# Kernel optimization log

Measured on AMD Instinct MI355X. Metric: run time of the kernel, lower is better.

The kernel has to match this reference:

```python
import jax, jax.numpy as jnp
import numpy as np
import math

HID = 128
NH = 8
HD = HID // NH
NL = 3
CLIP = 10.0
EPS = 1e-5

def _ln(x, g, b):
    mu = jnp.mean(x, axis=-1, keepdims=True)
    var = jnp.var(x, axis=-1, keepdims=True)
    return (x - mu) * jax.lax.rsqrt(var + EPS) * g + b

def _layer(h, e_bias1, e_gate2, g1, b1, wh, g2, b2, w1, w2):
    B, N, _ = h.shape
    h_in = h
    hn = _ln(h, g1, b1)
    qkv = hn @ wh                                   # (B,N,3H)
    q, k, v = jnp.split(qkv, 3, axis=-1)
    q = q.reshape(B, N, NH, HD).transpose(0, 2, 1, 3)  # (B,nh,N,hd)
    k = k.reshape(B, N, NH, HD).transpose(0, 2, 1, 3)
    v = v.reshape(B, N, NH, HD).transpose(0, 2, 1, 3)
    att = jnp.einsum('bhid,bhjd->bhij', q, k) * (1.0 / math.sqrt(HD))
    att = jax.nn.softmax(att + e_bias1, axis=-1) * e_gate2
    y = jnp.einsum('bhij,bhjd->bhid', att, v)
    y = y.transpose(0, 2, 1, 3).reshape(B, N, HID)
    z = _ln(y + h_in, g2, b2)
    mlp = jax.nn.relu(z @ w1) @ w2
    return mlp + y

def setup_inputs() -> dict:
    key = jax.random.key(0)
    ks = jax.random.split(key, 9)
    d = {
        'node_features': jax.random.normal(ks[0], (16, 256, 2), jnp.float32),
        'edge_features': jax.random.normal(ks[1], (16, 256, 256, 1), jnp.float32),
        'Wn': jax.random.normal(ks[2], (2, HID), jnp.float32) * 0.5,
        'We_in': jax.random.normal(ks[3], (1, HID), jnp.float32) * 0.1,
        'ln1_g': jnp.ones((NL, HID), jnp.float32),
        'ln1_b': jnp.zeros((NL, HID), jnp.float32),
        'Wh': jax.random.normal(ks[4], (NL, HID, 3 * HID), jnp.float32) * (1.0 / math.sqrt(HID)),
        'We': jax.random.normal(ks[5], (NL, HID, 2 * NH), jnp.float32) * (1.0 / math.sqrt(HID)),
        'ln2_g': jnp.ones((NL, HID), jnp.float32),
        'ln2_b': jnp.zeros((NL, HID), jnp.float32),
        'W1': jax.random.normal(ks[6], (NL, HID, 4 * HID), jnp.float32) * (1.0 / math.sqrt(HID)),
        'W2': jax.random.normal(ks[7], (NL, 4 * HID, HID), jnp.float32) * (1.0 / math.sqrt(4 * HID)),
        'Wdec': jax.random.normal(ks[8], (HID, 1), jnp.float32) * (1.0 / math.sqrt(HID)),
    }
    return d

def reference(node_features, edge_features, Wn, We_in, ln1_g, ln1_b, Wh, We, ln2_g, ln2_b, W1, W2, Wdec):
    h = node_features @ Wn                              # (B,N,H)
    e = edge_features @ We_in                           # (B,N,N,H)
    for i in range(NL):
        ee = e @ We[i]                                  # (B,N,N,2*nh)
        ee = ee.transpose(0, 3, 1, 2)                   # (B,2*nh,N,N)
        e1, e2 = ee[:, :NH], ee[:, NH:]
        h = _layer(h, e1, e2, ln1_g[i], ln1_b[i], Wh[i], ln2_g[i], ln2_b[i], W1[i], W2[i])
    out = h @ Wdec                                      # (B,N,1)
    out = CLIP * jnp.tanh(out / math.sqrt(HID))
    return out
```

## Files before the change

kernel.cpp:

```cpp
#include <hip/hip_runtime.h>
#include <math.h>

#define HID 128
#define NHEAD 8
#define NL 3
#define NS 256
#define ROWS 4096

typedef __attribute__((ext_vector_type(8))) short bf16x8;
typedef __attribute__((ext_vector_type(4))) float f32x4;

__device__ __forceinline__ float us2f(unsigned short s) { return __uint_as_float(((unsigned)s) << 16); }
__device__ __forceinline__ unsigned short f2b(float f) {
    unsigned u = __float_as_uint(f);
    return (unsigned short)((u + 0x7fff + ((u >> 16) & 1)) >> 16);
}

__global__ __launch_bounds__(256) void k_prep(
    const float* __restrict__ Wh, const float* __restrict__ W1, const float* __restrict__ W2,
    const float* __restrict__ We_in, const float* __restrict__ We,
    const float* __restrict__ nf, const float* __restrict__ Wn,
    unsigned short* __restrict__ WhH, unsigned short* __restrict__ WhL,
    unsigned short* __restrict__ W1H, unsigned short* __restrict__ W1L,
    unsigned short* __restrict__ W2H, unsigned short* __restrict__ W2L,
    float* __restrict__ sbuf, float* __restrict__ h)
{
    int b = blockIdx.x, t = threadIdx.x;
    if (b >= 529) {
        int idx = (b - 529) * 256 + t;
        int r = idx >> 7, c = idx & 127;
        h[idx] = nf[2 * r] * Wn[c] + nf[2 * r + 1] * Wn[HID + c];
        return;
    }
    if (b == 528) {
        if (t < NL * 2 * NHEAD) {
            int l = t / (2 * NHEAD), j = t % (2 * NHEAD);
            float acc = 0.f;
            for (int c = 0; c < HID; ++c)
                acc += We_in[c] * We[(long)(l * HID + c) * (2 * NHEAD) + j];
            sbuf[t] = acc;
        }
        return;
    }
    const float* S; unsigned short *OH, *OL; int K, N, kt, nt;
    if (b < 144) {
        int l = b / 48, rem = b % 48; kt = rem & 3; nt = rem >> 2; K = 128; N = 384;
        S = Wh + (long)l * 128 * 384; OH = WhH + (long)l * 384 * 128; OL = WhL + (long)l * 384 * 128;
    } else if (b < 336) {
        int b2 = b - 144; int l = b2 / 64, rem = b2 % 64; kt = rem & 3; nt = rem >> 2; K = 128; N = 512;
        S = W1 + (long)l * 128 * 512; OH = W1H + (long)l * 512 * 128; OL = W1L + (long)l * 512 * 128;
    } else {
        int b2 = b - 336; int l = b2 / 64, rem = b2 % 64; kt = rem & 15; nt = rem >> 4; K = 512; N = 128;
        S = W2 + (long)l * 512 * 128; OH = W2H + (long)l * 128 * 512; OL = W2L + (long)l * 128 * 512;
    }
    __shared__ float sm[32][33];
    int i0 = t >> 5, j = t & 31;
#pragma unroll
    for (int p = 0; p < 4; ++p) {
        int i = i0 + p * 8;
        sm[i][j] = S[(long)(kt * 32 + i) * N + nt * 32 + j];
    }
    __syncthreads();
#pragma unroll
    for (int p = 0; p < 4; ++p) {
        int n = i0 + p * 8;
        float v = sm[j][n];
        unsigned short hh = f2b(v);
        long o = (long)(nt * 32 + n) * K + kt * 32 + j;
        OH[o] = hh; OL[o] = f2b(v - us2f(hh));
    }
}

__global__ __launch_bounds__(256) void k_fgemm(
    const float* __restrict__ x, const float* __restrict__ x2,
    const float* __restrict__ g, const float* __restrict__ b,
    const unsigned short* __restrict__ WH, const unsigned short* __restrict__ WL,
    unsigned short* __restrict__ Ch, unsigned short* __restrict__ Cl,
    int mode)
{
    __shared__ unsigned short sAh[64 * 136], sAl[64 * 136];
    __shared__ unsigned short sWh[64 * 136], sWl[64 * 136];
    int t = threadIdx.x;
    int row0 = blockIdx.y * 64, col0 = blockIdx.x * 64;

#pragma unroll
    for (int p = 0; p < 4; ++p) {
        int rr = (t >> 4) + p * 16, ck = t & 15;
        *(uint4*)&sWh[rr * 136 + ck * 8] = *(const uint4*)&WH[(long)(col0 + rr) * 128 + ck * 8];
        *(uint4*)&sWl[rr * 136 + ck * 8] = *(const uint4*)&WL[(long)(col0 + rr) * 128 + ck * 8];
    }
#pragma unroll
    for (int pass = 0; pass < 2; ++pass) {
        int row = pass * 32 + (t >> 3);
        int p = t & 7, cb = p * 16;
        float v[16];
        const float* xp = x + (long)(row0 + row) * HID + cb;
#pragma unroll
        for (int j = 0; j < 16; j += 4) *(float4*)&v[j] = *(const float4*)(xp + j);
        if (x2) {
            const float* yp = x2 + (long)(row0 + row) * HID + cb;
#pragma unroll
            for (int j = 0; j < 16; j += 4) {
                float4 r4 = *(const float4*)(yp + j);
                v[j] += r4.x; v[j+1] += r4.y; v[j+2] += r4.z; v[j+3] += r4.w;
            }
        }
        float s = 0.f, s2 = 0.f;
#pragma unroll
        for (int j = 0; j < 16; ++j) { s += v[j]; s2 += v[j] * v[j]; }
        s  += __shfl_xor(s, 1);  s  += __shfl_xor(s, 2);  s  += __shfl_xor(s, 4);
        s2 += __shfl_xor(s2, 1); s2 += __shfl_xor(s2, 2); s2 += __shfl_xor(s2, 4);
        float mu  = s * (1.f / HID);
        float var = s2 * (1.f / HID) - mu * mu;
        float inv = rsqrtf(var + 1e-5f);
        unsigned short hi[16], lo[16];
#pragma unroll
        for (int j = 0; j < 16; ++j) {
            int c = cb + j;
            float o = (v[j] - mu) * inv * g[c] + b[c];
            hi[j] = f2b(o); lo[j] = f2b(o - us2f(hi[j]));
        }
        *(uint4*)&sAh[row * 136 + cb]     = *(uint4*)&hi[0];
        *(uint4*)&sAh[row * 136 + cb + 8] = *(uint4*)&hi[8];
        *(uint4*)&sAl[row * 136 + cb]     = *(uint4*)&lo[0];
        *(uint4*)&sAl[row * 136 + cb + 8] = *(uint4*)&lo[8];
    }
    __syncthreads();

    int w = t >> 6, lane = t & 63;
    int m = lane & 15, quad = lane >> 4;
    f32x4 acc[4];
#pragma unroll
    for (int i = 0; i < 4; ++i) acc[i] = (f32x4){0.f, 0.f, 0.f, 0.f};
#pragma unroll
    for (int c = 0; c < 4; ++c) {
        bf16x8 ah = *(const bf16x8*)&sAh[(w * 16 + m) * 136 + c * 32 + quad * 8];
        bf16x8 al = *(const bf16x8*)&sAl[(w * 16 + m) * 136 + c * 32 + quad * 8];
#pragma unroll
        for (int nt = 0; nt < 4; ++nt) {
            bf16x8 wh = *(const bf16x8*)&sWh[(nt * 16 + m) * 136 + c * 32 + quad * 8];
            bf16x8 wl = *(const bf16x8*)&sWl[(nt * 16 + m) * 136 + c * 32 + quad * 8];
            acc[nt] = __builtin_amdgcn_mfma_f32_16x16x32_bf16(ah, wh, acc[nt], 0, 0, 0);
            acc[nt] = __builtin_amdgcn_mfma_f32_16x16x32_bf16(ah, wl, acc[nt], 0, 0, 0);
            acc[nt] = __builtin_amdgcn_mfma_f32_16x16x32_bf16(al, wh, acc[nt], 0, 0, 0);
        }
    }
#pragma unroll
    for (int nt = 0; nt < 4; ++nt) {
        unsigned short hi4[4], lo4[4];
#pragma unroll
        for (int r = 0; r < 4; ++r) {
            float v = acc[nt][r];
            if (mode) v = fmaxf(v, 0.f);
            hi4[r] = f2b(v); lo4[r] = f2b(v - us2f(hi4[r]));
        }
        long o = (long)(col0 + nt * 16 + m) * ROWS + row0 + w * 16 + quad * 4;
        *(uint2*)&Ch[o] = *(const uint2*)hi4;
        *(uint2*)&Cl[o] = *(const uint2*)lo4;
    }
}

__global__ __launch_bounds__(512, 1) void k_mlp(
    const float* __restrict__ y, const float* __restrict__ h,
    const float* __restrict__ g, const float* __restrict__ b,
    const unsigned short* __restrict__ W1H_, const unsigned short* __restrict__ W1L_,
    const unsigned short* __restrict__ W2H_, const unsigned short* __restrict__ W2L_,
    float* __restrict__ hout, const float* __restrict__ Wdec, float* __restrict__ out)
{
    __shared__ __align__(16) unsigned short sAh[16 * 136], sAl[16 * 136];
    __shared__ __align__(16) unsigned short sHh[16 * 520], sHl[16 * 520];
    int t = threadIdx.x;
    int row0 = blockIdx.x * 16;
    int w = t >> 6, lane = t & 63;
    int m = lane & 15, quad = lane >> 4;

    const unsigned short* w1h = W1H_ + (long)(w * 64 + m) * 128 + quad * 8;
    const unsigned short* w1l = W1L_ + (long)(w * 64 + m) * 128 + quad * 8;
    bf16x8 p1h[4], p1l[4];
#pragma unroll
    for (int nt = 0; nt < 4; ++nt) {
        p1h[nt] = *(const bf16x8*)&w1h[nt * 16 * 128];
        p1l[nt] = *(const bf16x8*)&w1l[nt * 16 * 128];
    }

    {
        int row = t >> 5, cb = (t & 31) * 4;
        float4 a4 = *(const float4*)&y[(long)(row0 + row) * HID + cb];
        float4 b4 = *(const float4*)&h[(long)(row0 + row) * HID + cb];
        float v[4] = {a4.x + b4.x, a4.y + b4.y, a4.z + b4.z, a4.w + b4.w};
        float s = v[0] + v[1] + v[2] + v[3];
        float s2 = v[0]*v[0] + v[1]*v[1] + v[2]*v[2] + v[3]*v[3];
        s  += __shfl_xor(s, 1);  s  += __shfl_xor(s, 2);  s  += __shfl_xor(s, 4);
        s  += __shfl_xor(s, 8);  s  += __shfl_xor(s, 16);
        s2 += __shfl_xor(s2, 1); s2 += __shfl_xor(s2, 2); s2 += __shfl_xor(s2, 4);
        s2 += __shfl_xor(s2, 8); s2 += __shfl_xor(s2, 16);
        float mu  = s * (1.f / HID);
        float var = s2 * (1.f / HID) - mu * mu;
        float inv = rsqrtf(var + 1e-5f);
        unsigned short hi4[4], lo4[4];
#pragma unroll
        for (int j = 0; j < 4; ++j) {
            int c = cb + j;
            float o = (v[j] - mu) * inv * g[c] + b[c];
            hi4[j] = f2b(o); lo4[j] = f2b(o - us2f(hi4[j]));
        }
        *(uint2*)&sAh[row * 136 + cb] = *(const uint2*)hi4;
        *(uint2*)&sAl[row * 136 + cb] = *(const uint2*)lo4;
    }
    __syncthreads();

    f32x4 acc1[4];
#pragma unroll
    for (int i = 0; i < 4; ++i) acc1[i] = (f32x4){0.f, 0.f, 0.f, 0.f};
#pragma unroll
    for (int c = 0; c < 4; ++c) {
        bf16x8 ah = *(const bf16x8*)&sAh[m * 136 + c * 32 + quad * 8];
        bf16x8 al = *(const bf16x8*)&sAl[m * 136 + c * 32 + quad * 8];
#pragma unroll
        for (int nt = 0; nt < 4; ++nt) {
            bf16x8 wh = (c == 0) ? p1h[nt] : *(const bf16x8*)&w1h[nt * 16 * 128 + c * 32];
            bf16x8 wl = (c == 0) ? p1l[nt] : *(const bf16x8*)&w1l[nt * 16 * 128 + c * 32];
            acc1[nt] = __builtin_amdgcn_mfma_f32_16x16x32_bf16(wh, ah, acc1[nt], 0, 0, 0);
            acc1[nt] = __builtin_amdgcn_mfma_f32_16x16x32_bf16(wh, al, acc1[nt], 0, 0, 0);
            acc1[nt] = __builtin_amdgcn_mfma_f32_16x16x32_bf16(wl, ah, acc1[nt], 0, 0, 0);
        }
    }
#pragma unroll
    for (int nt = 0; nt < 4; ++nt) {
        unsigned short hi4[4], lo4[4];
#pragma unroll
        for (int r = 0; r < 4; ++r) {
            float v = fmaxf(acc1[nt][r], 0.f);
            hi4[r] = f2b(v);
            lo4[r] = f2b(v - us2f(hi4[r]));
        }
        int kk = w * 64 + nt * 16 + quad * 4;
        *(uint2*)&sHh[m * 520 + kk] = *(const uint2*)hi4;
        *(uint2*)&sHl[m * 520 + kk] = *(const uint2*)lo4;
    }

    const unsigned short* w2h = W2H_ + (long)(w * 16 + m) * 512 + quad * 8;
    const unsigned short* w2l = W2L_ + (long)(w * 16 + m) * 512 + quad * 8;
    bf16x8 p2h = *(const bf16x8*)w2h;
    bf16x8 p2l = *(const bf16x8*)w2l;
    __syncthreads();

    f32x4 acc2 = (f32x4){0.f, 0.f, 0.f, 0.f};
#pragma unroll
    for (int c = 0; c < 16; ++c) {
        bf16x8 ah = *(const bf16x8*)&sHh[m * 520 + c * 32 + quad * 8];
        bf16x8 al = *(const bf16x8*)&sHl[m * 520 + c * 32 + quad * 8];
        bf16x8 wh = (c == 0) ? p2h : *(const bf16x8*)&w2h[c * 32];
        bf16x8 wl = (c == 0) ? p2l : *(const bf16x8*)&w2l[c * 32];
        acc2 = __builtin_amdgcn_mfma_f32_16x16x32_bf16(ah, wh, acc2, 0, 0, 0);
        acc2 = __builtin_amdgcn_mfma_f32_16x16x32_bf16(ah, wl, acc2, 0, 0, 0);
        acc2 = __builtin_amdgcn_mfma_f32_16x16x32_bf16(al, wh, acc2, 0, 0, 0);
    }
    __syncthreads();
    float* ht = (float*)&sHh[0];
#pragma unroll
    for (int r = 0; r < 4; ++r) {
        int row = quad * 4 + r;
        int col = w * 16 + m;
        float v = acc2[r] + y[(long)(row0 + row) * HID + col];
        hout[(long)(row0 + row) * HID + col] = v;
        ht[row * 132 + col] = v;
    }
    __syncthreads();
    if (Wdec && t < 256) {
        int row = t >> 4, sub = t & 15;
        float vv[8];
        *(float4*)&vv[0] = *(const float4*)&ht[row * 132 + sub * 8];
        *(float4*)&vv[4] = *(const float4*)&ht[row * 132 + sub * 8 + 4];
        float a = 0.f;
#pragma unroll
        for (int j = 0; j < 8; ++j) a += vv[j] * Wdec[sub * 8 + j];
        a += __shfl_xor(a, 1); a += __shfl_xor(a, 2); a += __shfl_xor(a, 4); a += __shfl_xor(a, 8);
        if (sub == 0) out[row0 + row] = 10.f * tanhf(a * 0.08838834764831845f);
    }
}

#define PAS 268
#define KQS 20
__global__ __launch_bounds__(256) void k_attn(
    const unsigned short* __restrict__ qkvH, const unsigned short* __restrict__ qkvL,
    const float* __restrict__ ef, const float* __restrict__ sbuf,
    int layer, float* __restrict__ y)
{
    __shared__ unsigned short Kh[NS * KQS], Kl[NS * KQS];
    __shared__ unsigned short Qh[64 * KQS], Ql[64 * KQS];
    __shared__ unsigned short Vh[16 * PAS], Vl[16 * PAS];
    __shared__ unsigned short Pa[4][16 * PAS];
    int bid = blockIdx.x;
    int q4 = bid & 3, hh = (bid >> 2) & 7, bb = bid >> 5;
    int t = threadIdx.x;
    {
        int d = t >> 4, kc = (t & 15) * 16;
        long base = (long)ROWS * (HID + hh * 16 + d) + bb * NS + kc;
        long vbase = base + (long)ROWS * 128;
        union { uint4 u[2]; unsigned short s[16]; } KH, KL, VH, VL;
        KH.u[0] = *(const uint4*)&qkvH[base];      KH.u[1] = *(const uint4*)&qkvH[base + 8];
        KL.u[0] = *(const uint4*)&qkvL[base];      KL.u[1] = *(const uint4*)&qkvL[base + 8];
        VH.u[0] = *(const uint4*)&qkvH[vbase];     VH.u[1] = *(const uint4*)&qkvH[vbase + 8];
        VL.u[0] = *(const uint4*)&qkvL[vbase];     VL.u[1] = *(const uint4*)&qkvL[vbase + 8];
#pragma unroll
        for (int j = 0; j < 16; ++j) {
            Kh[(kc + j) * KQS + d] = KH.s[j];
            Kl[(kc + j) * KQS + d] = KL.s[j];
        }
#pragma unroll
        for (int j = 0; j < 4; ++j) {
            *(uint2*)&Vh[d * PAS + kc + j * 4] = *(const uint2*)&VH.s[j * 4];
            *(uint2*)&Vl[d * PAS + kc + j * 4] = *(const uint2*)&VL.s[j * 4];
        }
    }
    {
        int d = t >> 4, rc = (t & 15) * 4;
        long qb = (long)ROWS * (hh * 16 + d) + bb * NS + q4 * 64 + rc;
        union { uint2 u; unsigned short s[4]; } QH, QL;
        QH.u = *(const uint2*)&qkvH[qb];
        QL.u = *(const uint2*)&qkvL[qb];
#pragma unroll
        for (int j = 0; j < 4; ++j) {
            Qh[(rc + j) * KQS + d] = QH.s[j];
            Ql[(rc + j) * KQS + d] = QL.s[j];
        }
    }
    __syncthreads();
    int w = t >> 6, lane = t & 63;
    int m = lane & 15, quad = lane >> 4;
    float s1  = sbuf[layer * 16 + hh];
    float s2g = sbuf[layer * 16 + NHEAD + hh];
    unsigned short* Paw = Pa[w];

    bf16x8 qh = (bf16x8){0,0,0,0,0,0,0,0}, ql = qh;
    if (quad < 2) {
        qh = *(const bf16x8*)&Qh[(w * 16 + m) * KQS + quad * 8];
        ql = *(const bf16x8*)&Ql[(w * 16 + m) * KQS + quad * 8];
    }
    f32x4 sc[16];
#pragma unroll
    for (int ct = 0; ct < 16; ++ct) {
        bf16x8 kh = (bf16x8){0,0,0,0,0,0,0,0}, kl = kh;
        if (quad < 2) {
            kh = *(const bf16x8*)&Kh[(ct * 16 + m) * KQS + quad * 8];
            kl = *(const bf16x8*)&Kl[(ct * 16 + m) * KQS + quad * 8];
        }
        f32x4 a = (f32x4){0.f, 0.f, 0.f, 0.f};
        a = __builtin_amdgcn_mfma_f32_16x16x32_bf16(qh, kh, a, 0, 0, 0);
        a = __builtin_amdgcn_mfma_f32_16x16x32_bf16(qh, kl, a, 0, 0, 0);
        a = __builtin_amdgcn_mfma_f32_16x16x32_bf16(ql, kh, a, 0, 0, 0);
        sc[ct] = a;
    }
    int baserow = q4 * 64 + w * 16 + quad * 4;
    float s[4] = {0.f, 0.f, 0.f, 0.f};
#pragma unroll
    for (int ct = 0; ct < 16; ++ct) {
#pragma unroll
        for (int r = 0; r < 4; ++r) {
            float e = ef[((long)(bb * NS + baserow + r)) * NS + ct * 16 + m];
            float p = __expf(sc[ct][r] * 0.25f + e * s1);
            s[r] += p;
            Paw[(quad * 4 + r) * PAS + ct * 16 + m] = f2b(p * e);
        }
    }
    float inv[4];
#pragma unroll
    for (int r = 0; r < 4; ++r) {
        float ss = s[r];
        ss += __shfl_xor(ss, 1); ss += __shfl_xor(ss, 2);
        ss += __shfl_xor(ss, 4); ss += __shfl_xor(ss, 8);
        inv[r] = s2g / ss;
    }
    f32x4 acc = (f32x4){0.f, 0.f, 0.f, 0.f};
#pragma unroll
    for (int sft = 0; sft < 8; ++sft) {
        bf16x8 pf = *(const bf16x8*)&Paw[m * PAS + sft * 32 + quad * 8];
        bf16x8 vh = *(const bf16x8*)&Vh[m * PAS + sft * 32 + quad * 8];
        bf16x8 vl = *(const bf16x8*)&Vl[m * PAS + sft * 32 + quad * 8];
        acc = __builtin_amdgcn_mfma_f32_16x16x32_bf16(pf, vh, acc, 0, 0, 0);
        acc = __builtin_amdgcn_mfma_f32_16x16x32_bf16(pf, vl, acc, 0, 0, 0);
    }
#pragma unroll
    for (int r = 0; r < 4; ++r) {
        int row = q4 * 64 + w * 16 + quad * 4 + r;
        y[((long)(bb * NS + row)) * HID + hh * 16 + m] = acc[r] * inv[r];
    }
}

extern "C" void kernel_launch(void* const* d_in, const int* in_sizes, int n_in,
                              void* d_out, int out_size, void* d_ws, size_t ws_size,
                              hipStream_t stream) {
    const float* nf    = (const float*)d_in[0];
    const float* ef    = (const float*)d_in[1];
    const float* Wn    = (const float*)d_in[2];
    const float* We_in = (const float*)d_in[3];
    const float* ln1g  = (const float*)d_in[4];
    const float* ln1b  = (const float*)d_in[5];
    const float* Wh    = (const float*)d_in[6];
    const float* We    = (const float*)d_in[7];
    const float* ln2g  = (const float*)d_in[8];
    const float* ln2b  = (const float*)d_in[9];
    const float* W1    = (const float*)d_in[10];
    const float* W2    = (const float*)d_in[11];
    const float* Wdec  = (const float*)d_in[12];

    float* ws   = (float*)d_ws;
    float* sbuf = ws;
    float* h    = ws + 64;
    float* y    = h + ROWS * HID;
    unsigned short* qkvH = (unsigned short*)(y + ROWS * HID);
    unsigned short* qkvL = qkvH + (long)384 * ROWS;
    unsigned short* WhH  = qkvL + (long)384 * ROWS;
    unsigned short* WhL  = WhH + (long)NL * 384 * 128;
    unsigned short* W1H  = WhL + (long)NL * 384 * 128;
    unsigned short* W1L  = W1H + (long)NL * 512 * 128;
    unsigned short* W2H  = W1L + (long)NL * 512 * 128;
    unsigned short* W2L  = W2H + (long)NL * 128 * 512;

    k_prep<<<529 + ROWS * HID / 256, 256, 0, stream>>>(Wh, W1, W2, We_in, We, nf, Wn,
                                    WhH, WhL, W1H, W1L, W2H, W2L, sbuf, h);
    for (int l = 0; l < NL; ++l) {
        k_fgemm<<<dim3(6, 64), 256, 0, stream>>>(h, nullptr,
            ln1g + l * HID, ln1b + l * HID,
            WhH + (long)l * 384 * 128, WhL + (long)l * 384 * 128,
            qkvH, qkvL, 0);
        k_attn<<<512, 256, 0, stream>>>(qkvH, qkvL, ef, sbuf, l, y);
        int last = (l == NL - 1);
        k_mlp<<<ROWS / 16, 512, 0, stream>>>(y, h,
            ln2g + l * HID, ln2b + l * HID,
            W1H + (long)l * 512 * 128, W1L + (long)l * 512 * 128,
            W2H + (long)l * 128 * 512, W2L + (long)l * 128 * 512,
            h, last ? Wdec : nullptr, (float*)d_out);
    }
}
```

Measured before the change: 202.8 us.

## Pack split-bf16 QK MFMAs into K dimension, double-buffer W2 loads, vectorize h init

The QK^T score computation previously zero-padded half of the 32-wide K slot (head dim 16) and ran three MFMAs per tile. It now places the hi/lo split pieces into the two halves of K, so two MFMAs cover hi*hi + lo*hi + hi*lo + lo*lo. The MLP second GEMM prefetches W2 fragments two steps ahead using double-buffered registers, to hide global load latency. The initial node embedding in k_prep writes float4 values per thread, which cuts the grid size for that part by four.

```diff
diff --git a/kernel.cpp b/kernel.cpp
--- a/kernel.cpp
+++ b/kernel.cpp
@@ -27,9 +27,14 @@
 {
     int b = blockIdx.x, t = threadIdx.x;
     if (b >= 529) {
-        int idx = (b - 529) * 256 + t;
-        int r = idx >> 7, c = idx & 127;
-        h[idx] = nf[2 * r] * Wn[c] + nf[2 * r + 1] * Wn[HID + c];
+        int idx4 = (b - 529) * 256 + t;
+        int r = idx4 >> 5, c4 = (idx4 & 31) * 4;
+        float n0 = nf[2 * r], n1 = nf[2 * r + 1];
+        float4 w0 = *(const float4*)&Wn[c4];
+        float4 w1 = *(const float4*)&Wn[HID + c4];
+        float4 o = {n0 * w0.x + n1 * w1.x, n0 * w0.y + n1 * w1.y,
+                    n0 * w0.z + n1 * w1.z, n0 * w0.w + n1 * w1.w};
+        *(float4*)&h[idx4 * 4] = o;
         return;
     }
     if (b == 528) {
@@ -241,17 +246,21 @@
 
     const unsigned short* w2h = W2H_ + (long)(w * 16 + m) * 512 + quad * 8;
     const unsigned short* w2l = W2L_ + (long)(w * 16 + m) * 512 + quad * 8;
-    bf16x8 p2h = *(const bf16x8*)w2h;
-    bf16x8 p2l = *(const bf16x8*)w2l;
+    bf16x8 fh0 = *(const bf16x8*)w2h,        fl0 = *(const bf16x8*)w2l;
+    bf16x8 fh1 = *(const bf16x8*)&w2h[32],   fl1 = *(const bf16x8*)&w2l[32];
     __syncthreads();
 
     f32x4 acc2 = (f32x4){0.f, 0.f, 0.f, 0.f};
 #pragma unroll
     for (int c = 0; c < 16; ++c) {
+        bf16x8 wh = (c & 1) ? fh1 : fh0;
+        bf16x8 wl = (c & 1) ? fl1 : fl0;
+        if (c < 14) {
+            if (c & 1) { fh1 = *(const bf16x8*)&w2h[(c + 2) * 32]; fl1 = *(const bf16x8*)&w2l[(c + 2) * 32]; }
+            else       { fh0 = *(const bf16x8*)&w2h[(c + 2) * 32]; fl0 = *(const bf16x8*)&w2l[(c + 2) * 32]; }
+        }
         bf16x8 ah = *(const bf16x8*)&sHh[m * 520 + c * 32 + quad * 8];
         bf16x8 al = *(const bf16x8*)&sHl[m * 520 + c * 32 + quad * 8];
-        bf16x8 wh = (c == 0) ? p2h : *(const bf16x8*)&w2h[c * 32];
-        bf16x8 wl = (c == 0) ? p2l : *(const bf16x8*)&w2l[c * 32];
         acc2 = __builtin_amdgcn_mfma_f32_16x16x32_bf16(ah, wh, acc2, 0, 0, 0);
         acc2 = __builtin_amdgcn_mfma_f32_16x16x32_bf16(ah, wl, acc2, 0, 0, 0);
         acc2 = __builtin_amdgcn_mfma_f32_16x16x32_bf16(al, wh, acc2, 0, 0, 0);
@@ -333,23 +342,19 @@
     float s2g = sbuf[layer * 16 + NHEAD + hh];
     unsigned short* Paw = Pa[w];
 
-    bf16x8 qh = (bf16x8){0,0,0,0,0,0,0,0}, ql = qh;
-    if (quad < 2) {
-        qh = *(const bf16x8*)&Qh[(w * 16 + m) * KQS + quad * 8];
-        ql = *(const bf16x8*)&Ql[(w * 16 + m) * KQS + quad * 8];
-    }
+    const unsigned short* Qa = (quad < 2) ? Qh : Ql;
+    const unsigned short* Qb = (quad < 2) ? Ql : Qh;
+    const unsigned short* Ka = (quad < 2) ? Kh : Kl;
+    int qoff = (w * 16 + m) * KQS + (quad & 1) * 8;
+    bf16x8 qA = *(const bf16x8*)&Qa[qoff];
+    bf16x8 qB = *(const bf16x8*)&Qb[qoff];
     f32x4 sc[16];
 #pragma unroll
     for (int ct = 0; ct < 16; ++ct) {
-        bf16x8 kh = (bf16x8){0,0,0,0,0,0,0,0}, kl = kh;
-        if (quad < 2) {
-            kh = *(const bf16x8*)&Kh[(ct * 16 + m) * KQS + quad * 8];
-            kl = *(const bf16x8*)&Kl[(ct * 16 + m) * KQS + quad * 8];
-        }
+        bf16x8 kA = *(const bf16x8*)&Ka[(ct * 16 + m) * KQS + (quad & 1) * 8];
         f32x4 a = (f32x4){0.f, 0.f, 0.f, 0.f};
-        a = __builtin_amdgcn_mfma_f32_16x16x32_bf16(qh, kh, a, 0, 0, 0);
-        a = __builtin_amdgcn_mfma_f32_16x16x32_bf16(qh, kl, a, 0, 0, 0);
-        a = __builtin_amdgcn_mfma_f32_16x16x32_bf16(ql, kh, a, 0, 0, 0);
+        a = __builtin_amdgcn_mfma_f32_16x16x32_bf16(qA, kA, a, 0, 0, 0);
+        a = __builtin_amdgcn_mfma_f32_16x16x32_bf16(qB, kA, a, 0, 0, 0);
         sc[ct] = a;
     }
     int baserow = q4 * 64 + w * 16 + quad * 4;
@@ -418,7 +423,7 @@
     unsigned short* W2H  = W1L + (long)NL * 512 * 128;
     unsigned short* W2L  = W2H + (long)NL * 128 * 512;
 
-    k_prep<<<529 + ROWS * HID / 256, 256, 0, stream>>>(Wh, W1, W2, We_in, We, nf, Wn,
+    k_prep<<<529 + ROWS * HID / 1024, 256, 0, stream>>>(Wh, W1, W2, We_in, We, nf, Wn,
                                     WhH, WhL, W1H, W1L, W2H, W2L, sbuf, h);
     for (int l = 0; l < NL; ++l) {
         k_fgemm<<<dim3(6, 64), 256, 0, stream>>>(h, nullptr,
```

After: 210.2 us. 3.7% more time.
